# Kernel optimization log

Hardware: AMD Instinct MI355X
Metric: run time of the kernel (lower is better)

Reference implementation:

```python
import jax, jax.numpy as jnp
import numpy as np

N = 50000      # nodes
E = 600000     # edges
D = 128        # num_features == hidden_units
L = 4          # num_layers
C = 10         # num_classes
G = 512        # graphs in batch
BN_EPS = 1e-5


def setup_inputs() -> dict:
    key = jax.random.key(0)
    ks = jax.random.split(key, 10)
    x = jax.random.normal(ks[0], (N, D), dtype=jnp.float32)
    src = jax.random.randint(ks[1], (E,), 0, N)
    dst = jax.random.randint(ks[2], (E,), 0, N)
    edge_index = jnp.stack([src, dst]).astype(jnp.int64)
    batch = jnp.sort(jax.random.randint(ks[3], (N,), 0, G)).astype(jnp.int64)
    s = 1.0 / np.sqrt(D)
    Wc1 = jax.random.uniform(ks[4], (L, D, D), jnp.float32, -s, s)
    bc1 = jnp.zeros((L, D), jnp.float32)
    Wc2 = jax.random.uniform(ks[5], (L, D, D), jnp.float32, -s, s)
    bc2 = jnp.zeros((L, D), jnp.float32)
    g_mid = jnp.ones((L, D), jnp.float32)   # BN gamma inside conv MLP
    b_mid = jnp.zeros((L, D), jnp.float32)
    g_out = jnp.ones((L, D), jnp.float32)   # BN gamma after conv
    b_out = jnp.zeros((L, D), jnp.float32)
    fcW = jax.random.uniform(ks[6], (L + 1, D, C), jnp.float32, -s, s)
    fcb = jnp.zeros((L + 1, C), jnp.float32)
    return dict(x=x, edge_index=edge_index, batch=batch, Wc1=Wc1, bc1=bc1,
                Wc2=Wc2, bc2=bc2, g_mid=g_mid, b_mid=b_mid, g_out=g_out,
                b_out=b_out, fcW=fcW, fcb=fcb)


def _bn(h, gamma, beta):
    # training-mode BatchNorm1d over the node axis (biased variance)
    mu = h.mean(0)
    var = h.var(0)
    return (h - mu) * jax.lax.rsqrt(var + BN_EPS) * gamma + beta


def reference(x, edge_index, batch, Wc1, bc1, Wc2, bc2, g_mid, b_mid,
              g_out, b_out, fcW, fcb):
    src, dst = edge_index[0], edge_index[1]
    outs = [x]
    h = x
    for i in range(L):
        # GINConv (eps=0): nn( x + sum_{j in N(i)} x_j )
        agg = jax.ops.segment_sum(h[src], dst, num_segments=N)
        z = h + agg
        z = z @ Wc1[i] + bc1[i]
        z = jax.nn.relu(_bn(z, g_mid[i], b_mid[i]))
        z = z @ Wc2[i] + bc2[i]
        h = jax.nn.relu(_bn(z, g_out[i], b_out[i]))  # outer BN + ReLU
        outs.append(h)
    out = jnp.zeros((G, C), x.dtype)
    for i, o in enumerate(outs):
        pooled = jax.ops.segment_sum(o, batch, num_segments=G)  # [G, D]
        out = out + pooled @ fcW[i] + fcb[i]  # dropout p=0.0 -> identity
    return jax.nn.log_softmax(out, axis=-1)
```

## Files before the change

kernel.cpp:

```cpp
#include <hip/hip_runtime.h>
#include <hip/hip_bf16.h>

#define NN 50000
#define EE 600000
#define DD 128
#define LL 4
#define CC 10
#define GG 512
#define BN_EPS 1e-5f
#define ELLW 48

#define EB_BLOCKS ((EE + 255) / 256)
#define PW_BLOCKS ((8 * DD * DD) / 256)
#define GP_BLOCKS 3
#define AGG_BLOCKS ((NN + 3) / 4)
#define ZERO_N (8 * 256 + NN)
#define ZERO_BLOCKS ((ZERO_N + 255) / 256)

typedef __attribute__((ext_vector_type(8))) short short8;
typedef __attribute__((ext_vector_type(4))) float f32x4;

__device__ __forceinline__ unsigned short f2b(float f) {
    union { float f; unsigned int u; } v; v.f = f;
    unsigned int u = v.u;
    unsigned int r = (u + 0x7fffu + ((u >> 16) & 1u)) >> 16;
    return (unsigned short)r;
}
__device__ __forceinline__ float b2f(unsigned short h) {
    union { unsigned int u; float f; } v; v.u = ((unsigned int)h) << 16;
    return v.f;
}


__global__ __launch_bounds__(256) void zero_kernel(int* __restrict__ base) {
    int i = blockIdx.x * 256 + threadIdx.x;
    if (i < ZERO_N) base[i] = 0;
}


__global__ __launch_bounds__(256) void setup_kernel(const int* __restrict__ src,
                                                    const int* __restrict__ dst,
                                                    int* __restrict__ cursor,
                                                    unsigned short* __restrict__ ell,
                                                    const float* __restrict__ Wc1,
                                                    const float* __restrict__ Wc2,
                                                    unsigned short* __restrict__ WTb,
                                                    const int* __restrict__ batch,
                                                    int* __restrict__ gptr,
                                                    const float* __restrict__ x,
                                                    unsigned short* __restrict__ xb,
                                                    float* __restrict__ pooled0) {
    int b = blockIdx.x;
    if (b < EB_BLOCKS) {
        int e = b * 256 + threadIdx.x;
        if (e < EE) {
            int d = dst[e];
            int slot = atomicAdd(&cursor[d], 1);
            if (slot < ELLW) ell[(size_t)d * ELLW + slot] = (unsigned short)src[e];
        }
    } else if (b < EB_BLOCKS + PW_BLOCKS) {
        int idx = (b - EB_BLOCKS) * 256 + threadIdx.x;
        int mat = idx >> 14;
        int n = (idx >> 7) & 127;
        int k = idx & 127;
        const float* srcp = (mat < 4) ? (Wc1 + (size_t)mat * DD * DD)
                                      : (Wc2 + (size_t)(mat - 4) * DD * DD);
        WTb[idx] = f2b(srcp[k * DD + n]);
    } else if (b < EB_BLOCKS + PW_BLOCKS + GP_BLOCKS) {
        int g = (b - EB_BLOCKS - PW_BLOCKS) * 256 + threadIdx.x;
        if (g > GG) return;
        int lo = 0, hi = NN;
        while (lo < hi) {
            int mid = (lo + hi) >> 1;
            if (batch[mid] < g) lo = mid + 1; else hi = mid;
        }
        gptr[g] = lo;
    } else {
        __shared__ float2 red[4][64];
        const int g = b - EB_BLOCKS - PW_BLOCKS - GP_BLOCKS;
        int lo = 0, hi = NN;
        while (lo < hi) { int mid = (lo + hi) >> 1; if (batch[mid] < g) lo = mid + 1; else hi = mid; }
        int beg = lo;
        hi = NN;
        while (lo < hi) { int mid = (lo + hi) >> 1; if (batch[mid] < g + 1) lo = mid + 1; else hi = mid; }
        int end = lo;
        int wave = threadIdx.x >> 6, lane = threadIdx.x & 63;
        float ax = 0.f, ay = 0.f;
        for (int r = beg + wave; r < end; r += 4) {
            float2 v = ((const float2*)(x + (size_t)r * DD))[lane];
            ax += v.x; ay += v.y;
            ((unsigned int*)(xb + (size_t)r * DD))[lane] =
                (unsigned int)f2b(v.x) | ((unsigned int)f2b(v.y) << 16);
        }
        red[wave][lane] = make_float2(ax, ay);
        __syncthreads();
        if (threadIdx.x < 64) {
            float2 a = red[0][lane], bb = red[1][lane], c = red[2][lane], d = red[3][lane];
            ((float2*)pooled0)[(size_t)g * 64 + lane] =
                make_float2(a.x + bb.x + c.x + d.x, a.y + bb.y + c.y + d.y);
        }
    }
}


template <bool BN>
__device__ __forceinline__ void agg_node(int node, const unsigned short* __restrict__ hb,
                                         const unsigned short* __restrict__ ell,
                                         const int* __restrict__ degA,
                                         const float* __restrict__ stats,
                                         const float* __restrict__ gamma,
                                         const float* __restrict__ beta,
                                         unsigned short* __restrict__ outb) {
    const int lane = threadIdx.x & 63;
    const int seg = lane & 15;
    const int slot = lane >> 4;

    float A[8], B[8];
    if (BN) {
#pragma unroll
        for (int j = 0; j < 8; ++j) {
            int c = seg * 8 + j;
            float mu = stats[c] * (1.0f / NN);
            float var = stats[DD + c] * (1.0f / NN) - mu * mu;
            A[j] = gamma[c] * rsqrtf(var + BN_EPS);
            B[j] = beta[c] - mu * A[j];
        }
    }

    const uint4* hb4 = (const uint4*)hb;
    uint4 self = hb4[(size_t)node * 16 + seg];

    float acc[8];
#pragma unroll
    for (int j = 0; j < 8; ++j) acc[j] = 0.f;

    const unsigned short* row = ell + (size_t)node * ELLW;
    const int dg = min(degA[node], ELLW);
    for (int e = 0; e < dg; e += 16) {
        int idx[4];
        bool val[4];
#pragma unroll
        for (int i = 0; i < 4; ++i) {
            int t = e + i * 4 + slot;
            val[i] = (t < dg);
            idx[i] = row[val[i] ? t : 0];
        }
        uint4 v[4];
#pragma unroll
        for (int i = 0; i < 4; ++i) v[i] = hb4[(size_t)idx[i] * 16 + seg];
#pragma unroll
        for (int i = 0; i < 4; ++i) {
            if (val[i]) {
#pragma unroll
                for (int j = 0; j < 4; ++j) {
                    unsigned int u = ((unsigned int*)&v[i])[j];
                    float x = b2f((unsigned short)(u & 0xffff));
                    float y = b2f((unsigned short)(u >> 16));
                    if (BN) {
                        x = fmaxf(0.f, fmaf(x, A[2 * j], B[2 * j]));
                        y = fmaxf(0.f, fmaf(y, A[2 * j + 1], B[2 * j + 1]));
                    }
                    acc[2 * j] += x;
                    acc[2 * j + 1] += y;
                }
            }
        }
    }

#pragma unroll
    for (int j = 0; j < 8; ++j) {
        acc[j] += __shfl_xor(acc[j], 16);
        acc[j] += __shfl_xor(acc[j], 32);
    }

    if (slot == 0) {
        uint4 o;
#pragma unroll
        for (int j = 0; j < 4; ++j) {
            unsigned int u = ((unsigned int*)&self)[j];
            float x = b2f((unsigned short)(u & 0xffff));
            float y = b2f((unsigned short)(u >> 16));
            if (BN) {
                x = fmaxf(0.f, fmaf(x, A[2 * j], B[2 * j]));
                y = fmaxf(0.f, fmaf(y, A[2 * j + 1], B[2 * j + 1]));
            }
            ((unsigned int*)&o)[j] =
                (unsigned int)f2b(acc[2 * j] + x) | ((unsigned int)f2b(acc[2 * j + 1] + y) << 16);
        }
        ((uint4*)outb)[(size_t)node * 16 + seg] = o;
    }
}

__global__ __launch_bounds__(256) void aggregate_x(const unsigned short* __restrict__ hb,
                                                   const unsigned short* __restrict__ ell,
                                                   const int* __restrict__ degA,
                                                   unsigned short* __restrict__ outb) {
    int node = blockIdx.x * 4 + (threadIdx.x >> 6);
    if (node >= NN) return;
    agg_node<false>(node, hb, ell, degA, nullptr, nullptr, nullptr, outb);
}


__global__ __launch_bounds__(256, 2) void gemm_mfma(
    const unsigned short* __restrict__ Ab,
    const unsigned short* __restrict__ WTb,
    const float* __restrict__ bias,
    const float* __restrict__ bnStatsIn,
    const float* __restrict__ gamma, const float* __restrict__ beta,
    unsigned short* __restrict__ Outb,
    float* __restrict__ statsOut)
{
    __shared__ unsigned short As[128 * 128];
    __shared__ float AbnS[DD], BbnS[DD];
    __shared__ float colred[2][DD];

    const int tid = threadIdx.x;
    const int row0 = blockIdx.x * 128;
    const bool doBn = (bnStatsIn != nullptr);
    const int lane = tid & 63;
    const int fr = lane & 15, fq = lane >> 4;

    short8 bfrag[8][4];
#pragma unroll
    for (int n = 0; n < 8; ++n)
#pragma unroll
        for (int kk = 0; kk < 4; ++kk)
            bfrag[n][kk] = *(const short8*)((const char*)WTb + (n * 16 + fr) * 256 + kk * 64 + fq * 16);

    if (tid < DD) {
        colred[0][tid] = 0.f;
        colred[1][tid] = 0.f;
        if (doBn) {
            float mu = bnStatsIn[tid] * (1.0f / NN);
            float var = bnStatsIn[DD + tid] * (1.0f / NN) - mu * mu;
            float A = gamma[tid] * rsqrtf(var + BN_EPS);
            AbnS[tid] = A;
            BbnS[tid] = beta[tid] - mu * A;
        }
    }
    if (doBn) __syncthreads();

#pragma unroll
    for (int i = 0; i < 8; ++i) {
        int c = tid + i * 256;
        int row = c >> 4, seg = c & 15;
        int gr = row0 + row;
        uint4 v = make_uint4(0u, 0u, 0u, 0u);
        if (gr < NN) v = ((const uint4*)(Ab + (size_t)gr * DD))[seg];
        if (doBn) {
            int k0 = seg * 8;
#pragma unroll
            for (int e = 0; e < 4; ++e) {
                unsigned int u = ((unsigned int*)&v)[e];
                int cidx = k0 + 2 * e;
                float lo = fmaxf(0.f, fmaf(b2f((unsigned short)(u & 0xffff)), AbnS[cidx], BbnS[cidx]));
                float hi = fmaxf(0.f, fmaf(b2f((unsigned short)(u >> 16)), AbnS[cidx + 1], BbnS[cidx + 1]));
                ((unsigned int*)&v)[e] = (unsigned int)f2b(lo) | ((unsigned int)f2b(hi) << 16);
            }
        }
        int byte = (row * 256 + seg * 16) ^ ((row & 7) << 4);
        *(uint4*)((char*)As + byte) = v;
    }
    __syncthreads();

    const int wave = tid >> 6;
    const int wr0 = wave * 32;

    f32x4 acc[2][8];
#pragma unroll
    for (int m = 0; m < 2; ++m)
#pragma unroll
        for (int n = 0; n < 8; ++n) acc[m][n] = (f32x4)0.f;

#pragma unroll
    for (int kk = 0; kk < 4; ++kk) {
        int kbyte = kk * 64 + fq * 16;
        short8 a[2];
#pragma unroll
        for (int m = 0; m < 2; ++m) {
            int row = wr0 + m * 16 + fr;
            a[m] = *(const short8*)((const char*)As + ((row * 256 + kbyte) ^ ((row & 7) << 4)));
        }
#pragma unroll
        for (int m = 0; m < 2; ++m)
#pragma unroll
            for (int n = 0; n < 8; ++n)
                acc[m][n] = __builtin_amdgcn_mfma_f32_16x16x32_bf16(a[m], bfrag[n][kk], acc[m][n], 0, 0, 0);
    }

    float bias_n[8], s[8], q[8];
#pragma unroll
    for (int n = 0; n < 8; ++n) {
        bias_n[n] = bias[n * 16 + fr];
        s[n] = 0.f;
        q[n] = 0.f;
    }
#pragma unroll
    for (int m = 0; m < 2; ++m) {
        int rbase = row0 + wr0 + m * 16 + fq * 4;
#pragma unroll
        for (int j = 0; j < 4; ++j) {
            int gr = rbase + j;
            if (gr < NN) {
#pragma unroll
                for (int n = 0; n < 8; ++n) {
                    float o = acc[m][n][j] + bias_n[n];
                    Outb[(size_t)gr * DD + n * 16 + fr] = f2b(o);
                    s[n] += o;
                    q[n] += o * o;
                }
            }
        }
    }
#pragma unroll
    for (int n = 0; n < 8; ++n) {
        s[n] += __shfl_xor(s[n], 16);
        s[n] += __shfl_xor(s[n], 32);
        q[n] += __shfl_xor(q[n], 16);
        q[n] += __shfl_xor(q[n], 32);
    }
    if (fq == 0) {
#pragma unroll
        for (int n = 0; n < 8; ++n) {
            atomicAdd(&colred[0][n * 16 + fr], s[n]);
            atomicAdd(&colred[1][n * 16 + fr], q[n]);
        }
    }
    __syncthreads();
    if (tid < DD) {
        atomicAdd(&statsOut[tid], colred[0][tid]);
        atomicAdd(&statsOut[DD + tid], colred[1][tid]);
    }
}


template <bool LAST>
__global__ __launch_bounds__(256) void post_layer(
    const unsigned short* __restrict__ Z,
    const float* __restrict__ stats,
    const float* __restrict__ gamma,
    const float* __restrict__ beta,
    const int* __restrict__ gptr,
    const unsigned short* __restrict__ ell,
    const int* __restrict__ degA,
    float* __restrict__ pooledDst,
    unsigned short* __restrict__ aggOut,
    const float* __restrict__ pooledAll,
    const float* __restrict__ fcW,
    const float* __restrict__ fcb,
    float* __restrict__ out)
{
    const int bid = blockIdx.x;
    if (bid < GG) {
        __shared__ float2 red[4][64];
        __shared__ float p4[DD];
        const int g = bid;
        const int wave = threadIdx.x >> 6, lane = threadIdx.x & 63;
        const int c0 = lane * 2, c1 = c0 + 1;
        float mu0 = stats[c0] * (1.0f / NN);
        float var0 = stats[DD + c0] * (1.0f / NN) - mu0 * mu0;
        float A0 = gamma[c0] * rsqrtf(var0 + BN_EPS);
        float B0 = beta[c0] - mu0 * A0;
        float mu1 = stats[c1] * (1.0f / NN);
        float var1 = stats[DD + c1] * (1.0f / NN) - mu1 * mu1;
        float A1 = gamma[c1] * rsqrtf(var1 + BN_EPS);
        float B1 = beta[c1] - mu1 * A1;

        float ax = 0.f, ay = 0.f;
        int beg = gptr[g], end = gptr[g + 1];
        for (int r = beg + wave; r < end; r += 4) {
            unsigned int u = ((const unsigned int*)(Z + (size_t)r * DD))[lane];
            ax += fmaxf(0.f, fmaf(b2f((unsigned short)(u & 0xffff)), A0, B0));
            ay += fmaxf(0.f, fmaf(b2f((unsigned short)(u >> 16)), A1, B1));
        }
        red[wave][lane] = make_float2(ax, ay);
        __syncthreads();
        if (threadIdx.x < 64) {
            float2 a = red[0][lane], b = red[1][lane], c = red[2][lane], d = red[3][lane];
            float2 r2 = make_float2(a.x + b.x + c.x + d.x, a.y + b.y + c.y + d.y);
            ((float2*)pooledDst)[(size_t)g * 64 + lane] = r2;
            if (LAST) {
                p4[c0] = r2.x;
                p4[c1] = r2.y;
            }
        }
        if (LAST) {
            __syncthreads();
            if (threadIdx.x < 64) {
                float acc[CC];
#pragma unroll
                for (int c = 0; c < CC; ++c) acc[c] = 0.f;
                for (int i = 0; i < LL + 1; ++i) {
                    const float* Wf = fcW + (size_t)i * DD * CC;
                    for (int k = lane; k < DD; k += 64) {
                        float pv = (i == LL) ? p4[k] : pooledAll[((size_t)i * GG + g) * DD + k];
                        const float* wr = Wf + k * CC;
#pragma unroll
                        for (int c = 0; c < CC; ++c) acc[c] = fmaf(pv, wr[c], acc[c]);
                    }
                }
#pragma unroll
                for (int c = 0; c < CC; ++c)
                    for (int off = 32; off > 0; off >>= 1) acc[c] += __shfl_down(acc[c], off);
                if (lane == 0) {
#pragma unroll
                    for (int c = 0; c < CC; ++c) {
                        float b = 0.f;
                        for (int i = 0; i < LL + 1; ++i) b += fcb[i * CC + c];
                        acc[c] += b;
                    }
                    float m = acc[0];
#pragma unroll
                    for (int c = 1; c < CC; ++c) m = fmaxf(m, acc[c]);
                    float se = 0.f;
#pragma unroll
                    for (int c = 0; c < CC; ++c) se += expf(acc[c] - m);
                    float lse = m + logf(se);
#pragma unroll
                    for (int c = 0; c < CC; ++c) out[(size_t)g * CC + c] = acc[c] - lse;
                }
            }
        }
    } else {
        int node = (bid - GG) * 4 + (threadIdx.x >> 6);
        if (node >= NN) return;
        agg_node<true>(node, Z, ell, degA, stats, gamma, beta, aggOut);
    }
}


extern "C" void kernel_launch(void* const* d_in, const int* in_sizes, int n_in,
                              void* d_out, int out_size, void* d_ws, size_t ws_size,
                              hipStream_t stream) {
    const float* x     = (const float*)d_in[0];
    const int*   ei    = (const int*)d_in[1];
    const int*   batch = (const int*)d_in[2];
    const float* Wc1   = (const float*)d_in[3];
    const float* bc1   = (const float*)d_in[4];
    const float* Wc2   = (const float*)d_in[5];
    const float* bc2   = (const float*)d_in[6];
    const float* g_mid = (const float*)d_in[7];
    const float* b_mid = (const float*)d_in[8];
    const float* g_out = (const float*)d_in[9];
    const float* b_out = (const float*)d_in[10];
    const float* fcW   = (const float*)d_in[11];
    const float* fcb   = (const float*)d_in[12];
    float* out = (float*)d_out;

    char* p = (char*)d_ws;
    unsigned short* xb   = (unsigned short*)p; p += (size_t)NN * DD * 2;
    unsigned short* aggb = (unsigned short*)p; p += (size_t)NN * DD * 2;
    unsigned short* z1b  = (unsigned short*)p; p += (size_t)NN * DD * 2;
    unsigned short* z2b  = (unsigned short*)p; p += (size_t)NN * DD * 2;
    unsigned short* WTb  = (unsigned short*)p; p += (size_t)8 * DD * DD * 2;
    float* pooled = (float*)p; p += (size_t)(LL + 1) * GG * DD * 4;
    float* statb  = (float*)p; p += 8 * 256 * 4;
    int* cursor = (int*)p; p += (size_t)NN * 4;
    unsigned short* ell = (unsigned short*)p; p += (size_t)NN * ELLW * 2;
    int* gptr   = (int*)p; p += (size_t)(GG + 16) * 4;

    const int* src = ei;
    const int* dst = ei + EE;

    zero_kernel<<<ZERO_BLOCKS, 256, 0, stream>>>((int*)statb);
    setup_kernel<<<EB_BLOCKS + PW_BLOCKS + GP_BLOCKS + GG, 256, 0, stream>>>(
        src, dst, cursor, ell, Wc1, Wc2, WTb, batch, gptr, x, xb, pooled);

    const int gemmGrid = (NN + 127) / 128;
    aggregate_x<<<AGG_BLOCKS, 256, 0, stream>>>(xb, ell, cursor, aggb);
    for (int l = 0; l < LL; ++l) {
        gemm_mfma<<<gemmGrid, 256, 0, stream>>>(
            aggb, WTb + (size_t)l * DD * DD, bc1 + (size_t)l * DD,
            nullptr, nullptr, nullptr,
            z1b, statb + (size_t)(2 * l) * 256);
        gemm_mfma<<<gemmGrid, 256, 0, stream>>>(
            z1b, WTb + (size_t)(4 + l) * DD * DD, bc2 + (size_t)l * DD,
            statb + (size_t)(2 * l) * 256, g_mid + (size_t)l * DD, b_mid + (size_t)l * DD,
            z2b, statb + (size_t)(2 * l + 1) * 256);
        if (l < LL - 1) {
            post_layer<false><<<GG + AGG_BLOCKS, 256, 0, stream>>>(
                z2b, statb + (size_t)(2 * l + 1) * 256,
                g_out + (size_t)l * DD, b_out + (size_t)l * DD,
                gptr, ell, cursor,
                pooled + (size_t)(l + 1) * GG * DD, aggb,
                nullptr, nullptr, nullptr, nullptr);
        } else {
            post_layer<true><<<GG, 256, 0, stream>>>(
                z2b, statb + (size_t)(2 * l + 1) * 256,
                g_out + (size_t)l * DD, b_out + (size_t)l * DD,
                gptr, ell, cursor,
                pooled + (size_t)(l + 1) * GG * DD, nullptr,
                pooled, fcW, fcb, out);
        }
    }
}
```

Measured before the change: 371.4 us.

## Aggregate two nodes per wavefront and store ELL neighbour indices as int

Each wavefront now aggregates a pair of adjacent nodes. Their neighbour gathers are interleaved so more independent loads are in flight, and the loop runs to the larger of the two degrees. The ELL table changes from 16-bit to 32-bit indices, which also fixes truncation of node ids above 65535, at the cost of twice the index memory. The setup kernel reorders its block roles so the per-graph pooling blocks come first. Row reads for t beyond the valid degree may now touch padded entries that were never written, but those values are masked before use.

Result: faster. 359.5 us (-3.2%).

```diff
diff --git a/kernel.cpp b/kernel.cpp
--- a/kernel.cpp
+++ b/kernel.cpp
@@ -13,7 +13,7 @@
 #define EB_BLOCKS ((EE + 255) / 256)
 #define PW_BLOCKS ((8 * DD * DD) / 256)
 #define GP_BLOCKS 3
-#define AGG_BLOCKS ((NN + 3) / 4)
+#define AGG_BLOCKS (NN / 8)
 #define ZERO_N (8 * 256 + NN)
 #define ZERO_BLOCKS ((ZERO_N + 255) / 256)
 
@@ -41,7 +41,7 @@
 __global__ __launch_bounds__(256) void setup_kernel(const int* __restrict__ src,
                                                     const int* __restrict__ dst,
                                                     int* __restrict__ cursor,
-                                                    unsigned short* __restrict__ ell,
+                                                    int* __restrict__ ell,
                                                     const float* __restrict__ Wc1,
                                                     const float* __restrict__ Wc2,
                                                     unsigned short* __restrict__ WTb,
@@ -51,33 +51,9 @@
                                                     unsigned short* __restrict__ xb,
                                                     float* __restrict__ pooled0) {
     int b = blockIdx.x;
-    if (b < EB_BLOCKS) {
-        int e = b * 256 + threadIdx.x;
-        if (e < EE) {
-            int d = dst[e];
-            int slot = atomicAdd(&cursor[d], 1);
-            if (slot < ELLW) ell[(size_t)d * ELLW + slot] = (unsigned short)src[e];
-        }
-    } else if (b < EB_BLOCKS + PW_BLOCKS) {
-        int idx = (b - EB_BLOCKS) * 256 + threadIdx.x;
-        int mat = idx >> 14;
-        int n = (idx >> 7) & 127;
-        int k = idx & 127;
-        const float* srcp = (mat < 4) ? (Wc1 + (size_t)mat * DD * DD)
-                                      : (Wc2 + (size_t)(mat - 4) * DD * DD);
-        WTb[idx] = f2b(srcp[k * DD + n]);
-    } else if (b < EB_BLOCKS + PW_BLOCKS + GP_BLOCKS) {
-        int g = (b - EB_BLOCKS - PW_BLOCKS) * 256 + threadIdx.x;
-        if (g > GG) return;
-        int lo = 0, hi = NN;
-        while (lo < hi) {
-            int mid = (lo + hi) >> 1;
-            if (batch[mid] < g) lo = mid + 1; else hi = mid;
-        }
-        gptr[g] = lo;
-    } else {
+    if (b < GG) {
         __shared__ float2 red[4][64];
-        const int g = b - EB_BLOCKS - PW_BLOCKS - GP_BLOCKS;
+        const int g = b;
         int lo = 0, hi = NN;
         while (lo < hi) { int mid = (lo + hi) >> 1; if (batch[mid] < g) lo = mid + 1; else hi = mid; }
         int beg = lo;
@@ -99,13 +75,37 @@
             ((float2*)pooled0)[(size_t)g * 64 + lane] =
                 make_float2(a.x + bb.x + c.x + d.x, a.y + bb.y + c.y + d.y);
         }
+    } else if (b < GG + EB_BLOCKS) {
+        int e = (b - GG) * 256 + threadIdx.x;
+        if (e < EE) {
+            int d = dst[e];
+            int slot = atomicAdd(&cursor[d], 1);
+            if (slot < ELLW) ell[(size_t)d * ELLW + slot] = src[e];
+        }
+    } else if (b < GG + EB_BLOCKS + PW_BLOCKS) {
+        int idx = (b - GG - EB_BLOCKS) * 256 + threadIdx.x;
+        int mat = idx >> 14;
+        int n = (idx >> 7) & 127;
+        int k = idx & 127;
+        const float* srcp = (mat < 4) ? (Wc1 + (size_t)mat * DD * DD)
+                                      : (Wc2 + (size_t)(mat - 4) * DD * DD);
+        WTb[idx] = f2b(srcp[k * DD + n]);
+    } else {
+        int g = (b - GG - EB_BLOCKS - PW_BLOCKS) * 256 + threadIdx.x;
+        if (g > GG) return;
+        int lo = 0, hi = NN;
+        while (lo < hi) {
+            int mid = (lo + hi) >> 1;
+            if (batch[mid] < g) lo = mid + 1; else hi = mid;
+        }
+        gptr[g] = lo;
     }
 }
 
 
 template <bool BN>
-__device__ __forceinline__ void agg_node(int node, const unsigned short* __restrict__ hb,
-                                         const unsigned short* __restrict__ ell,
+__device__ __forceinline__ void agg_pair(int nA, const unsigned short* __restrict__ hb,
+                                         const int* __restrict__ ell,
                                          const int* __restrict__ degA,
                                          const float* __restrict__ stats,
                                          const float* __restrict__ gamma,
@@ -128,52 +128,80 @@
     }
 
     const uint4* hb4 = (const uint4*)hb;
-    uint4 self = hb4[(size_t)node * 16 + seg];
-
-    float acc[8];
-#pragma unroll
-    for (int j = 0; j < 8; ++j) acc[j] = 0.f;
-
-    const unsigned short* row = ell + (size_t)node * ELLW;
-    const int dg = min(degA[node], ELLW);
-    for (int e = 0; e < dg; e += 16) {
-        int idx[4];
-        bool val[4];
+    uint4 self = hb4[(size_t)(nA + (slot == 1 ? 1 : 0)) * 16 + seg];
+
+    float accA[8], accB[8];
+#pragma unroll
+    for (int j = 0; j < 8; ++j) { accA[j] = 0.f; accB[j] = 0.f; }
+
+    const int* rowA = ell + (size_t)nA * ELLW;
+    const int* rowB = rowA + ELLW;
+    const int dgA = min(degA[nA], ELLW);
+    const int dgB = min(degA[nA + 1], ELLW);
+    const int dgM = max(dgA, dgB);
+
+    for (int e = 0; e < dgM; e += 16) {
+        bool vA[4], vB[4];
+        int iA[4], iB[4];
 #pragma unroll
         for (int i = 0; i < 4; ++i) {
             int t = e + i * 4 + slot;
-            val[i] = (t < dg);
-            idx[i] = row[val[i] ? t : 0];
-        }
-        uint4 v[4];
-#pragma unroll
-        for (int i = 0; i < 4; ++i) v[i] = hb4[(size_t)idx[i] * 16 + seg];
+            vA[i] = (t < dgA);
+            vB[i] = (t < dgB);
+            iA[i] = rowA[t];
+            iB[i] = rowB[t];
+        }
+        uint4 a[4], b[4];
 #pragma unroll
         for (int i = 0; i < 4; ++i) {
-            if (val[i]) {
+            if (vA[i]) a[i] = hb4[(size_t)iA[i] * 16 + seg];
+        }
+#pragma unroll
+        for (int i = 0; i < 4; ++i) {
+            if (vB[i]) b[i] = hb4[(size_t)iB[i] * 16 + seg];
+        }
+#pragma unroll
+        for (int i = 0; i < 4; ++i) {
+            if (vA[i]) {
 #pragma unroll
                 for (int j = 0; j < 4; ++j) {
-                    unsigned int u = ((unsigned int*)&v[i])[j];
+                    unsigned int u = ((unsigned int*)&a[i])[j];
                     float x = b2f((unsigned short)(u & 0xffff));
                     float y = b2f((unsigned short)(u >> 16));
                     if (BN) {
                         x = fmaxf(0.f, fmaf(x, A[2 * j], B[2 * j]));
                         y = fmaxf(0.f, fmaf(y, A[2 * j + 1], B[2 * j + 1]));
                     }
-                    acc[2 * j] += x;
-                    acc[2 * j + 1] += y;
+                    accA[2 * j] += x;
+                    accA[2 * j + 1] += y;
                 }
             }
+            if (vB[i]) {
+#pragma unroll
+                for (int j = 0; j < 4; ++j) {
+                    unsigned int u = ((unsigned int*)&b[i])[j];
+                    float x = b2f((unsigned short)(u & 0xffff));
+                    float y = b2f((unsigned short)(u >> 16));
+                    if (BN) {
+                        x = fmaxf(0.f, fmaf(x, A[2 * j], B[2 * j]));
+                        y = fmaxf(0.f, fmaf(y, A[2 * j + 1], B[2 * j + 1]));
+                    }
+                    accB[2 * j] += x;
+                    accB[2 * j + 1] += y;
+                }
+            }
         }
     }
 
 #pragma unroll
     for (int j = 0; j < 8; ++j) {
-        acc[j] += __shfl_xor(acc[j], 16);
-        acc[j] += __shfl_xor(acc[j], 32);
-    }
-
-    if (slot == 0) {
+        accA[j] += __shfl_xor(accA[j], 16);
+        accA[j] += __shfl_xor(accA[j], 32);
+        accB[j] += __shfl_xor(accB[j], 16);
+        accB[j] += __shfl_xor(accB[j], 32);
+    }
+
+    if (slot < 2) {
         uint4 o;
 #pragma unroll
         for (int j = 0; j < 4; ++j) {
@@ -184,20 +212,21 @@
                 x = fmaxf(0.f, fmaf(x, A[2 * j], B[2 * j]));
                 y = fmaxf(0.f, fmaf(y, A[2 * j + 1], B[2 * j + 1]));
             }
+            float sx = (slot == 0) ? accA[2 * j] : accB[2 * j];
+            float sy = (slot == 0) ? accA[2 * j + 1] : accB[2 * j + 1];
             ((unsigned int*)&o)[j] =
-                (unsigned int)f2b(acc[2 * j] + x) | ((unsigned int)f2b(acc[2 * j + 1] + y) << 16);
-        }
-        ((uint4*)outb)[(size_t)node * 16 + seg] = o;
+                (unsigned int)f2b(sx + x) | ((unsigned int)f2b(sy + y) << 16);
+        }
+        ((uint4*)outb)[(size_t)(nA + slot) * 16 + seg] = o;
     }
 }
 
 __global__ __launch_bounds__(256) void aggregate_x(const unsigned short* __restrict__ hb,
-                                                   const unsigned short* __restrict__ ell,
+                                                   const int* __restrict__ ell,
                                                    const int* __restrict__ degA,
                                                    unsigned short* __restrict__ outb) {
-    int node = blockIdx.x * 4 + (threadIdx.x >> 6);
-    if (node >= NN) return;
-    agg_node<false>(node, hb, ell, degA, nullptr, nullptr, nullptr, outb);
+    int nA = blockIdx.x * 8 + (threadIdx.x >> 6) * 2;
+    agg_pair<false>(nA, hb, ell, degA, nullptr, nullptr, nullptr, outb);
 }
 
 
@@ -341,7 +370,7 @@
     const float* __restrict__ gamma,
     const float* __restrict__ beta,
     const int* __restrict__ gptr,
-    const unsigned short* __restrict__ ell,
+    const int* __restrict__ ell,
     const int* __restrict__ degA,
     float* __restrict__ pooledDst,
     unsigned short* __restrict__ aggOut,
@@ -422,9 +451,8 @@
             }
         }
     } else {
-        int node = (bid - GG) * 4 + (threadIdx.x >> 6);
-        if (node >= NN) return;
-        agg_node<true>(node, Z, ell, degA, stats, gamma, beta, aggOut);
+        int nA = (bid - GG) * 8 + (threadIdx.x >> 6) * 2;
+        agg_pair<true>(nA, Z, ell, degA, stats, gamma, beta, aggOut);
     }
 }
 
@@ -456,14 +484,14 @@
     float* pooled = (float*)p; p += (size_t)(LL + 1) * GG * DD * 4;
     float* statb  = (float*)p; p += 8 * 256 * 4;
     int* cursor = (int*)p; p += (size_t)NN * 4;
-    unsigned short* ell = (unsigned short*)p; p += (size_t)NN * ELLW * 2;
+    int* ell    = (int*)p; p += (size_t)NN * ELLW * 4;
     int* gptr   = (int*)p; p += (size_t)(GG + 16) * 4;
 
     const int* src = ei;
     const int* dst = ei + EE;
 
     zero_kernel<<<ZERO_BLOCKS, 256, 0, stream>>>((int*)statb);
-    setup_kernel<<<EB_BLOCKS + PW_BLOCKS + GP_BLOCKS + GG, 256, 0, stream>>>(
+    setup_kernel<<<GG + EB_BLOCKS + PW_BLOCKS + GP_BLOCKS, 256, 0, stream>>>(
         src, dst, cursor, ell, Wc1, Wc2, WTb, batch, gptr, x, xb, pooled);
 
     const int gemmGrid = (NN + 127) / 128;
```
